# Performance work log

Measured on AMD Instinct MI355X. Metric: run time of the kernel, lower is better.

The kernel has to match this reference:

```python
import jax, jax.numpy as jnp
import numpy as np

T, B, H = 32768, 32, 64


def setup_inputs() -> dict:
    key = jax.random.key(0)
    ks = jax.random.split(key, 7)
    s = 1.0 / np.sqrt(H)  # PyTorch LSTM init scale
    return {
        "x": jax.random.normal(ks[0], (T, B, 1), dtype=jnp.float32),
        "W_ih": jax.random.uniform(ks[1], (4 * H, 1), minval=-s, maxval=s, dtype=jnp.float32),
        "W_hh": jax.random.uniform(ks[2], (4 * H, H), minval=-s, maxval=s, dtype=jnp.float32),
        "b_ih": jax.random.uniform(ks[3], (4 * H,), minval=-s, maxval=s, dtype=jnp.float32),
        "b_hh": jax.random.uniform(ks[4], (4 * H,), minval=-s, maxval=s, dtype=jnp.float32),
        "W_out": jax.random.uniform(ks[5], (1, H), minval=-s, maxval=s, dtype=jnp.float32),
        "b_out": jax.random.uniform(ks[6], (1,), minval=-s, maxval=s, dtype=jnp.float32),
    }


def reference(x, W_ih, W_hh, b_ih, b_hh, W_out, b_out):
    # x: [T, B, 1]; single-layer LSTM (PyTorch gate order i, f, g, o), zero initial state.
    Tn, Bn, _ = x.shape
    Hn = W_hh.shape[1]
    # precompute input contribution to gates: [T, B, 4H]
    xg = jnp.einsum('tbi,gi->tbg', x, W_ih) + b_ih + b_hh

    def step(carry, xg_t):
        h, c = carry
        gates = xg_t + h @ W_hh.T  # [B, 4H]
        i, f, g, o = jnp.split(gates, 4, axis=-1)
        i = jax.nn.sigmoid(i)
        f = jax.nn.sigmoid(f)
        g = jnp.tanh(g)
        o = jax.nn.sigmoid(o)
        c = f * c + i * g
        h = o * jnp.tanh(c)
        return (h, c), h

    h0 = jnp.zeros((Bn, Hn), dtype=x.dtype)
    c0 = jnp.zeros((Bn, Hn), dtype=x.dtype)
    _, hs = jax.lax.scan(step, (h0, c0), xg)  # hs: [T, B, H]
    out = jnp.einsum('tbh,oh->tbo', hs, W_out) + b_out
    return out + x
```

## Files before the change

kernel.cpp:

```cpp
#include <hip/hip_runtime.h>

#define TT 32768
#define BB 32

typedef _Float16 half2_t __attribute__((ext_vector_type(2)));
union H2U { half2_t h2; unsigned u; _Float16 h[2]; };

static __device__ __forceinline__ unsigned packh2(float a, float b) {
    H2U t; t.h[0] = (_Float16)a; t.h[1] = (_Float16)b; return t.u;
}
static __device__ __forceinline__ float fdot2u(unsigned wu, unsigned hu, float acc) {
    H2U w, h; w.u = wu; h.u = hu;
    return __builtin_amdgcn_fdot2(w.h2, h.h2, acc, false);
}
static __device__ __forceinline__ float rlanef(float v, int lane) {
    return __uint_as_float((unsigned)__builtin_amdgcn_readlane((int)__float_as_uint(v), lane));
}
template <int CTRL>
static __device__ __forceinline__ float dppf(float v) {
    return __uint_as_float((unsigned)__builtin_amdgcn_mov_dpp(
        (int)__float_as_uint(v), CTRL, 0xF, 0xF, true));
}
static __device__ __forceinline__ float exp2_raw(float x) {
    float r; asm("v_exp_f32 %0, %1" : "=v"(r) : "v"(x)); return r;
}

__global__ __attribute__((amdgpu_waves_per_eu(1, 1))) __launch_bounds__(256)
void lstm_fused(
    const float* __restrict__ x,
    const float* __restrict__ W_ih,
    const float* __restrict__ W_hh,
    const float* __restrict__ b_ih,
    const float* __restrict__ b_hh,
    const float* __restrict__ W_out,
    const float* __restrict__ b_out,
    float* __restrict__ out)
{
    const int b   = blockIdx.x;
    const int tid = threadIdx.x;
    const int w   = tid >> 6;
    const int l   = tid & 63;
    const int g   = l & 3;
    const int n   = 16 * w + (l >> 2);

    __shared__ _Float16 hbuf[2][64];
    __shared__ float    pbuf[64][65];

    const float L2E = 1.4426950408889634f;
    const float si  = (g == 2) ? (-2.f * L2E) : (-L2E);
    const float nm_out = (g == 0) ? (-2.f * L2E) : ((g == 2) ? 2.f : 1.f);
    const float na     = (g == 2) ? -1.f : 0.f;

    unsigned wgp[32];
    #pragma unroll
    for (int j = 0; j < 16; ++j) {
        const float4 v = *reinterpret_cast<const float4*>(&W_hh[(g * 64 + n) * 64 + 4 * j]);
        wgp[2 * j]     = packh2(si * v.x, si * v.y);
        wgp[2 * j + 1] = packh2(si * v.z, si * v.w);
    }
    const float wih  = si * W_ih[g * 64 + n];
    const float bias = si * (b_ih[g * 64 + n] + b_hh[g * 64 + n]);
    const float wo_n = W_out[n];
    const float bo   = b_out[0];

    float c = 0.f;

    if (tid < 64) { ((unsigned*)hbuf)[tid & 31] = 0u; }
    if (tid < 64) { ((unsigned*)hbuf)[32 + (tid & 31)] = 0u; }
    float xwin  = x[(size_t)l * BB + b];
    float xnext = 0.f;
    __syncthreads();

    #pragma unroll 1
    for (int t = 0; t < TT; ++t) {
        const int s  = t & 63;
        const int rp = t & 1;

        if (s == 0) {
            int idx = t + 64 + l; if (idx > TT - 1) idx = TT - 1;
            xnext = x[(size_t)idx * BB + b];
        }
        const float xv = rlanef(xwin, s);

        float a0 = fmaf(xv, wih, bias), a1 = 0.f, a2 = 0.f, a3 = 0.f;
        const unsigned* hb = reinterpret_cast<const unsigned*>(&hbuf[rp][0]);
        #pragma unroll
        for (int r = 0; r < 8; ++r) {
            const uint4 hv = *reinterpret_cast<const uint4*>(&hb[4 * r]);
            a0 = fdot2u(wgp[4 * r + 0], hv.x, a0);
            a1 = fdot2u(wgp[4 * r + 1], hv.y, a1);
            a2 = fdot2u(wgp[4 * r + 2], hv.z, a2);
            a3 = fdot2u(wgp[4 * r + 3], hv.w, a3);
        }
        const float pre = (a0 + a1) + (a2 + a3);
        const float gv = fmaf(__builtin_amdgcn_rcpf(1.f + exp2_raw(pre)), nm_out, na);

        const float fv = dppf<0x55>(gv);
        const float gg = dppf<0xAA>(gv);
        const float ov = dppf<0xFF>(gv);

        c = fmaf(fv, c, gv * gg);
        const float th = fmaf(__builtin_amdgcn_rcpf(1.f + exp2_raw(c)), 2.f, -1.f);
        const float hn = ov * th;

        if (g == 0) {
            hbuf[rp ^ 1][n] = (_Float16)hn;
            pbuf[s][n]      = hn * wo_n;
        }

        if (s == 63) { asm volatile("s_waitcnt lgkmcnt(0)" ::: "memory"); }
        else         { asm volatile("s_waitcnt lgkmcnt(1)" ::: "memory"); }
        __builtin_amdgcn_s_barrier();
        __builtin_amdgcn_sched_barrier(0);

        if (s == 63) {
            const int c0 = g * 16;
            float s0 = 0.f, s1 = 0.f, s2 = 0.f, s3 = 0.f;
            #pragma unroll
            for (int j2 = 0; j2 < 4; ++j2) {
                const float4 v = *reinterpret_cast<const float4*>(&pbuf[n][c0 + 4 * j2]);
                s0 += v.x; s1 += v.y; s2 += v.z; s3 += v.w;
            }
            float sum = (s0 + s1) + (s2 + s3);
            sum += dppf<0xB1>(sum);
            sum += dppf<0x4E>(sum);
            const float xr = __uint_as_float((unsigned)__builtin_amdgcn_ds_bpermute(
                4 * n, (int)__float_as_uint(xwin)));
            if (g == 0) {
                const int tt = (t & ~63) + n;
                out[(size_t)tt * BB + b] = sum + bo + xr;
            }
            xwin = xnext;
        }
    }
}

extern "C" void kernel_launch(void* const* d_in, const int* in_sizes, int n_in,
                              void* d_out, int out_size, void* d_ws, size_t ws_size,
                              hipStream_t stream) {
    (void)in_sizes; (void)n_in; (void)d_ws; (void)ws_size; (void)out_size;
    const float* x    = (const float*)d_in[0];
    const float* wih  = (const float*)d_in[1];
    const float* whh  = (const float*)d_in[2];
    const float* bih  = (const float*)d_in[3];
    const float* bhh  = (const float*)d_in[4];
    const float* wout = (const float*)d_in[5];
    const float* bout = (const float*)d_in[6];
    hipLaunchKernelGGL(lstm_fused, dim3(BB), dim3(256), 0, stream,
                       x, wih, whh, bih, bhh, wout, bout, (float*)d_out);
}
```

Baseline: 10.41 ms.

## Split hidden-dimension dot products across lane pairs with 512-thread blocks

Each gate row's 64-element recurrent dot product is now split across two lanes, each holding 32 weights. The two partial sums are combined with a DPP row shift, and the block doubles to 512 threads (8 waves). The aim is to shorten the per-timestep serial dot-product chain and halve the LDS reads per thread. In exchange, every step's barrier now spans twice as many waves, the partial-wait lgkmcnt trick is replaced by a full wait, and the final tanh/h computation is folded into a single fma.

```diff
diff --git a/kernel.cpp b/kernel.cpp
--- a/kernel.cpp
+++ b/kernel.cpp
@@ -25,8 +25,7 @@
     float r; asm("v_exp_f32 %0, %1" : "=v"(r) : "v"(x)); return r;
 }
 
-__global__ __attribute__((amdgpu_waves_per_eu(1, 1))) __launch_bounds__(256)
-void lstm_fused(
+__global__ __launch_bounds__(512, 2) void lstm_fused(
     const float* __restrict__ x,
     const float* __restrict__ W_ih,
     const float* __restrict__ W_hh,
@@ -41,7 +40,8 @@
     const int w   = tid >> 6;
     const int l   = tid & 63;
     const int g   = l & 3;
-    const int n   = 16 * w + (l >> 2);
+    const int kh  = (l >> 2) & 1;
+    const int n   = 8 * w + (l >> 3);
 
     __shared__ _Float16 hbuf[2][64];
     __shared__ float    pbuf[64][65];
@@ -51,22 +51,22 @@
     const float nm_out = (g == 0) ? (-2.f * L2E) : ((g == 2) ? 2.f : 1.f);
     const float na     = (g == 2) ? -1.f : 0.f;
 
-    unsigned wgp[32];
+    unsigned wgp[16];
     #pragma unroll
-    for (int j = 0; j < 16; ++j) {
-        const float4 v = *reinterpret_cast<const float4*>(&W_hh[(g * 64 + n) * 64 + 4 * j]);
+    for (int j = 0; j < 8; ++j) {
+        const float4 v = *reinterpret_cast<const float4*>(
+            &W_hh[(g * 64 + n) * 64 + 32 * kh + 4 * j]);
         wgp[2 * j]     = packh2(si * v.x, si * v.y);
         wgp[2 * j + 1] = packh2(si * v.z, si * v.w);
     }
-    const float wih  = si * W_ih[g * 64 + n];
-    const float bias = si * (b_ih[g * 64 + n] + b_hh[g * 64 + n]);
+    const float wih  = (kh == 0) ? si * W_ih[g * 64 + n] : 0.f;
+    const float bias = (kh == 0) ? si * (b_ih[g * 64 + n] + b_hh[g * 64 + n]) : 0.f;
     const float wo_n = W_out[n];
     const float bo   = b_out[0];
 
     float c = 0.f;
 
-    if (tid < 64) { ((unsigned*)hbuf)[tid & 31] = 0u; }
-    if (tid < 64) { ((unsigned*)hbuf)[32 + (tid & 31)] = 0u; }
+    if (tid < 64) ((unsigned*)hbuf)[tid] = 0u;
     float xwin  = x[(size_t)l * BB + b];
     float xnext = 0.f;
     __syncthreads();
@@ -83,51 +83,56 @@
         const float xv = rlanef(xwin, s);
 
         float a0 = fmaf(xv, wih, bias), a1 = 0.f, a2 = 0.f, a3 = 0.f;
-        const unsigned* hb = reinterpret_cast<const unsigned*>(&hbuf[rp][0]);
-        #pragma unroll
-        for (int r = 0; r < 8; ++r) {
-            const uint4 hv = *reinterpret_cast<const uint4*>(&hb[4 * r]);
-            a0 = fdot2u(wgp[4 * r + 0], hv.x, a0);
-            a1 = fdot2u(wgp[4 * r + 1], hv.y, a1);
-            a2 = fdot2u(wgp[4 * r + 2], hv.z, a2);
-            a3 = fdot2u(wgp[4 * r + 3], hv.w, a3);
+        const unsigned* hb = reinterpret_cast<const unsigned*>(&hbuf[rp][0]) + 16 * kh;
+        {
+            const uint4 h0 = *reinterpret_cast<const uint4*>(hb);
+            const uint4 h1 = *reinterpret_cast<const uint4*>(hb + 4);
+            const uint4 h2 = *reinterpret_cast<const uint4*>(hb + 8);
+            const uint4 h3 = *reinterpret_cast<const uint4*>(hb + 12);
+            a0 = fdot2u(wgp[0],  h0.x, a0); a1 = fdot2u(wgp[1],  h0.y, a1);
+            a2 = fdot2u(wgp[2],  h0.z, a2); a3 = fdot2u(wgp[3],  h0.w, a3);
+            a0 = fdot2u(wgp[4],  h1.x, a0); a1 = fdot2u(wgp[5],  h1.y, a1);
+            a2 = fdot2u(wgp[6],  h1.z, a2); a3 = fdot2u(wgp[7],  h1.w, a3);
+            a0 = fdot2u(wgp[8],  h2.x, a0); a1 = fdot2u(wgp[9],  h2.y, a1);
+            a2 = fdot2u(wgp[10], h2.z, a2); a3 = fdot2u(wgp[11], h2.w, a3);
+            a0 = fdot2u(wgp[12], h3.x, a0); a1 = fdot2u(wgp[13], h3.y, a1);
+            a2 = fdot2u(wgp[14], h3.z, a2); a3 = fdot2u(wgp[15], h3.w, a3);
         }
-        const float pre = (a0 + a1) + (a2 + a3);
-        const float gv = fmaf(__builtin_amdgcn_rcpf(1.f + exp2_raw(pre)), nm_out, na);
+        const float ph  = (a0 + a1) + (a2 + a3);
+        const float pre = ph + dppf<0x104>(ph);
+        const float gv  = fmaf(__builtin_amdgcn_rcpf(1.f + exp2_raw(pre)), nm_out, na);
 
         const float fv = dppf<0x55>(gv);
         const float gg = dppf<0xAA>(gv);
         const float ov = dppf<0xFF>(gv);
 
         c = fmaf(fv, c, gv * gg);
-        const float th = fmaf(__builtin_amdgcn_rcpf(1.f + exp2_raw(c)), 2.f, -1.f);
-        const float hn = ov * th;
+        const float rc = __builtin_amdgcn_rcpf(1.f + exp2_raw(c));
+        const float hn = fmaf(2.f * ov, rc, -ov);
 
-        if (g == 0) {
+        if ((l & 7) == 0) {
             hbuf[rp ^ 1][n] = (_Float16)hn;
             pbuf[s][n]      = hn * wo_n;
         }
 
-        if (s == 63) { asm volatile("s_waitcnt lgkmcnt(0)" ::: "memory"); }
-        else         { asm volatile("s_waitcnt lgkmcnt(1)" ::: "memory"); }
+        asm volatile("s_waitcnt lgkmcnt(0)" ::: "memory");
         __builtin_amdgcn_s_barrier();
-        __builtin_amdgcn_sched_barrier(0);
+        asm volatile("" ::: "memory");
 
         if (s == 63) {
-            const int c0 = g * 16;
-            float s0 = 0.f, s1 = 0.f, s2 = 0.f, s3 = 0.f;
-            #pragma unroll
-            for (int j2 = 0; j2 < 4; ++j2) {
-                const float4 v = *reinterpret_cast<const float4*>(&pbuf[n][c0 + 4 * j2]);
-                s0 += v.x; s1 += v.y; s2 += v.z; s3 += v.w;
-            }
-            float sum = (s0 + s1) + (s2 + s3);
+            const int r  = 8 * w + (l >> 3);
+            const int c8 = (l & 7) * 8;
+            const float4 v0 = *reinterpret_cast<const float4*>(&pbuf[r][c8]);
+            const float4 v1 = *reinterpret_cast<const float4*>(&pbuf[r][c8 + 4]);
+            float sum = ((v0.x + v0.y) + (v0.z + v0.w)) +
+                        ((v1.x + v1.y) + (v1.z + v1.w));
             sum += dppf<0xB1>(sum);
             sum += dppf<0x4E>(sum);
+            sum += dppf<0x104>(sum);
             const float xr = __uint_as_float((unsigned)__builtin_amdgcn_ds_bpermute(
-                4 * n, (int)__float_as_uint(xwin)));
-            if (g == 0) {
-                const int tt = (t & ~63) + n;
+                4 * r, (int)__float_as_uint(xwin)));
+            if ((l & 7) == 0) {
+                const int tt = (t & ~63) + r;
                 out[(size_t)tt * BB + b] = sum + bo + xr;
             }
             xwin = xnext;
@@ -146,6 +151,6 @@
     const float* bhh  = (const float*)d_in[4];
     const float* wout = (const float*)d_in[5];
     const float* bout = (const float*)d_in[6];
-    hipLaunchKernelGGL(lstm_fused, dim3(BB), dim3(256), 0, stream,
+    hipLaunchKernelGGL(lstm_fused, dim3(BB), dim3(512), 0, stream,
                        x, wih, whh, bih, bhh, wout, bout, (float*)d_out);
 }
```

New measurement: 10.20 ms. 1.02x faster.
